# Optimization experiments

Measured on AMD Instinct MI355X. Metric: run time of the kernel, lower is better.

The kernel has to match this reference:

```python
import jax, jax.numpy as jnp
import numpy as np

N_ATOM = 2048
C_ATOM = 128
C_PAIR = 16
N_HEADS = 4
BLOCK = 128
EPS = 1e-5


def _layernorm(x):
    mu = jnp.mean(x, axis=-1, keepdims=True)
    var = jnp.mean(jnp.square(x - mu), axis=-1, keepdims=True)
    return (x - mu) / jnp.sqrt(var + EPS)


def setup_inputs() -> dict:
    key = jax.random.key(0)
    ks = jax.random.split(key, 12)
    s = 0.02
    x = jax.random.normal(ks[0], (N_ATOM, C_ATOM), jnp.float32)
    pair_emb = jax.random.normal(ks[1], (N_ATOM, N_ATOM, C_PAIR), jnp.float32)
    block_index = jax.random.randint(ks[2], (N_ATOM, BLOCK), 0, N_ATOM, jnp.int64)
    Wq = jax.random.normal(ks[3], (C_ATOM, C_ATOM), jnp.float32) * s
    Wk = jax.random.normal(ks[4], (C_ATOM, C_ATOM), jnp.float32) * s
    Wv = jax.random.normal(ks[5], (C_ATOM, C_ATOM), jnp.float32) * s
    Wb = jax.random.normal(ks[6], (N_HEADS, 1), jnp.float32) * s  # nn.Linear(1, num_heads)
    Wout = jax.random.normal(ks[7], (C_ATOM, C_ATOM), jnp.float32) * s
    W1 = jax.random.normal(ks[8], (4 * C_ATOM, C_ATOM), jnp.float32) * s
    b1 = jnp.zeros((4 * C_ATOM,), jnp.float32)
    W2 = jax.random.normal(ks[9], (C_ATOM, 4 * C_ATOM), jnp.float32) * s
    b2 = jnp.zeros((C_ATOM,), jnp.float32)
    return {"x": x, "pair_emb": pair_emb, "block_index": block_index,
            "Wq": Wq, "Wk": Wk, "Wv": Wv, "Wb": Wb, "Wout": Wout,
            "W1": W1, "b1": b1, "W2": W2, "b2": b2}


def reference(x, pair_emb, block_index, Wq, Wk, Wv, Wb, Wout, W1, b1, W2, b2):
    N = x.shape[0]
    d_head = C_ATOM // N_HEADS
    h = _layernorm(x)
    q = (h @ Wq.T).reshape(N, N_HEADS, d_head)
    k = (h @ Wk.T).reshape(N, N_HEADS, d_head)
    v = (h @ Wv.T).reshape(N, N_HEADS, d_head)

    # pair bias per head: mean over c_pair, then Linear(1 -> n_heads)
    pair_mean = jnp.mean(pair_emb, axis=-1)              # [N, N]
    pair_bias = pair_mean[..., None] * Wb[:, 0]          # [N, N, H]

    # local block-sparse attention: each query i attends to keys block_index[i]
    k_g = k[block_index]                                 # [N, B, H, d]
    v_g = v[block_index]                                 # [N, B, H, d]
    rows = jnp.arange(N)[:, None]
    bias = pair_bias[rows, block_index]                  # [N, B, H]

    scale = 1.0 / jnp.sqrt(jnp.asarray(d_head, q.dtype))
    scores = jnp.einsum('nhd,nbhd->nhb', q, k_g) * scale + jnp.transpose(bias, (0, 2, 1))
    attn = jax.nn.softmax(scores, axis=-1)               # [N, H, B]
    attn_out = jnp.einsum('nhb,nbhd->nhd', attn, v_g).reshape(N, C_ATOM)

    x = x + attn_out @ Wout.T
    h2 = _layernorm(x)
    mlp = jax.nn.silu(h2 @ W1.T + b1) @ W2.T + b2
    return x + mlp
```

## Files before the change

### kernel.cpp

```cpp
#include <hip/hip_runtime.h>
#include <hip/hip_bf16.h>

#define N_ATOMS 2048
#define C_DIM   128
#define C_PAIR  16
#define BLK_K   128
#define LN_EPS  1e-5f

typedef float f32x4 __attribute__((ext_vector_type(4)));
typedef short s16x8 __attribute__((ext_vector_type(8)));

__device__ __forceinline__ float bf_lo(unsigned int p) {
    union { unsigned int i; float f; } u; u.i = p << 16; return u.f;
}
__device__ __forceinline__ float bf_hi(unsigned int p) {
    union { unsigned int i; float f; } u; u.i = p & 0xffff0000u; return u.f;
}
__device__ __forceinline__ float bf2f(unsigned short s) {
    union { unsigned int i; float f; } u; u.i = ((unsigned int)s) << 16; return u.f;
}
__device__ __forceinline__ unsigned short f2bf(float f) {
    union { float f; unsigned int i; } u; u.f = f;
    const unsigned int r = u.i + 0x7fffu + ((u.i >> 16) & 1u);
    return (unsigned short)(r >> 16);
}

__device__ __forceinline__ s16x8 lda_frag(const unsigned short* base,
                                          int rowBytes, int kstep, int lane) {
    const int m    = lane & 15;
    const int koff = kstep * 64 + ((lane >> 4) << 4);
    const int addr = m * rowBytes + (koff ^ ((m & 7) << 4));
    return *reinterpret_cast<const s16x8*>(
        reinterpret_cast<const char*>(base) + addr);
}

__device__ void pack_unit(int u, int lane,
                          const float* __restrict__ Wout,
                          const float* __restrict__ W1,
                          const float* __restrict__ W2,
                          unsigned short* __restrict__ WoutP,
                          unsigned short* __restrict__ W1P,
                          unsigned short* __restrict__ W2P)
{
    const float* W; unsigned short* P; int K, local;
    if (u < 32)       { W = Wout; P = WoutP; K = 128; local = u; }
    else if (u < 160) { W = W1;   P = W1P;   K = 128; local = u - 32; }
    else              { W = W2;   P = W2P;   K = 512; local = u - 160; }
    const int ksteps = K >> 5;
    const int ntile  = local / ksteps;
    const int kstep  = local - ntile * ksteps;
    const int n  = ntile * 16 + (lane & 15);
    const int k0 = kstep * 32 + ((lane >> 4) << 3);
    const float4* src = reinterpret_cast<const float4*>(W + (size_t)n * K + k0);
    const float4 a = src[0], b = src[1];
    s16x8 o;
    o[0] = (short)f2bf(a.x); o[1] = (short)f2bf(a.y);
    o[2] = (short)f2bf(a.z); o[3] = (short)f2bf(a.w);
    o[4] = (short)f2bf(b.x); o[5] = (short)f2bf(b.y);
    o[6] = (short)f2bf(b.z); o[7] = (short)f2bf(b.w);
    reinterpret_cast<s16x8*>(P)[local * 64 + lane] = o;
}

__global__ __launch_bounds__(512) void ln_qkv_kernel(
    const float* __restrict__ x,
    const float* __restrict__ Wq, const float* __restrict__ Wk,
    const float* __restrict__ Wv,
    const float* __restrict__ Wout, const float* __restrict__ W1,
    const float* __restrict__ W2,
    float* __restrict__ q,
    unsigned short* __restrict__ kb, unsigned short* __restrict__ vb,
    unsigned short* __restrict__ WoutP, unsigned short* __restrict__ W1P,
    unsigned short* __restrict__ W2P)
{
    __shared__ __align__(16) unsigned short hB[16][128];
    const int t = threadIdx.x;
    const int bid = blockIdx.x;
    const int row0 = bid * 16;

    if (t < 64)       pack_unit(bid * 2,     t,       Wout, W1, W2, WoutP, W1P, W2P);
    else if (t < 128) pack_unit(bid * 2 + 1, t - 64,  Wout, W1, W2, WoutP, W1P, W2P);
    else if (t < 192 && bid < 32)
                      pack_unit(256 + bid,   t - 128, Wout, W1, W2, WoutP, W1P, W2P);

    {
        const int r = t >> 5, l = t & 31;
        const float4 xv = reinterpret_cast<const float4*>(
            x + (size_t)(row0 + r) * C_DIM)[l];
        float s  = xv.x + xv.y + xv.z + xv.w;
        float ss = xv.x*xv.x + xv.y*xv.y + xv.z*xv.z + xv.w*xv.w;
        #pragma unroll
        for (int m = 16; m >= 1; m >>= 1) {
            s  += __shfl_xor(s,  m);
            ss += __shfl_xor(ss, m);
        }
        const float mu  = s * (1.0f / 128.0f);
        const float var = ss * (1.0f / 128.0f) - mu * mu;
        const float inv = rsqrtf(var + LN_EPS);
        union { unsigned long long u64; unsigned short u16[4]; } pk;
        pk.u16[0] = f2bf((xv.x - mu) * inv);
        pk.u16[1] = f2bf((xv.y - mu) * inv);
        pk.u16[2] = f2bf((xv.z - mu) * inv);
        pk.u16[3] = f2bf((xv.w - mu) * inv);
        *reinterpret_cast<unsigned long long*>(
            reinterpret_cast<char*>(&hB[0][0]) +
            r * 256 + ((l * 8) ^ ((r & 7) << 4))) = pk.u64;
    }
    __syncthreads();

    {
        const int wv = t >> 6, lane = t & 63;
        s16x8 afr[4];
        #pragma unroll
        for (int ks = 0; ks < 4; ++ks) afr[ks] = lda_frag(&hB[0][0], 256, ks, lane);

        const int n = wv * 16 + (lane & 15);
        #pragma unroll
        for (int p = 0; p < 3; ++p) {
            const float* W = (p == 0) ? Wq : (p == 1) ? Wk : Wv;
            f32x4 acc = {0.f, 0.f, 0.f, 0.f};
            #pragma unroll
            for (int ks = 0; ks < 4; ++ks) {
                const int k0 = ks * 32 + ((lane >> 4) << 3);
                const float4* src = reinterpret_cast<const float4*>(
                    W + (size_t)n * C_DIM + k0);
                const float4 a = src[0], b = src[1];
                s16x8 bfr;
                bfr[0] = (short)f2bf(a.x); bfr[1] = (short)f2bf(a.y);
                bfr[2] = (short)f2bf(a.z); bfr[3] = (short)f2bf(a.w);
                bfr[4] = (short)f2bf(b.x); bfr[5] = (short)f2bf(b.y);
                bfr[6] = (short)f2bf(b.z); bfr[7] = (short)f2bf(b.w);
                acc = __builtin_amdgcn_mfma_f32_16x16x32_bf16(afr[ks], bfr, acc, 0, 0, 0);
            }
            #pragma unroll
            for (int ii = 0; ii < 4; ++ii) {
                const int m = ((lane >> 4) << 2) + ii;
                const size_t off = (size_t)(row0 + m) * C_DIM + n;
                if (p == 0)      q[off]  = acc[ii];
                else if (p == 1) kb[off] = f2bf(acc[ii]);
                else             vb[off] = f2bf(acc[ii]);
            }
        }
    }
}

__global__ __launch_bounds__(512, 4) void attn_mlp_kernel(
    const float* __restrict__ q, const unsigned short* __restrict__ kb,
    const unsigned short* __restrict__ vb, const float* __restrict__ pair,
    const int*  __restrict__ bidx, const float* __restrict__ Wb,
    const float* __restrict__ x,
    const unsigned short* __restrict__ WoutP,
    const unsigned short* __restrict__ W1P, const float* __restrict__ b1,
    const unsigned short* __restrict__ W2P, const float* __restrict__ b2,
    float* __restrict__ out)
{
    __shared__ __align__(16) float qS[4][128];
    __shared__ __align__(16) int   idxS[4][128];
    __shared__ __align__(16) float S[4][4][128];
    __shared__ __align__(16) float ys[4][128];
    __shared__ __align__(16) unsigned short aoB[16][128];
    __shared__ __align__(16) unsigned short h2B[16][128];
    __shared__ __align__(16) unsigned short gsB[16][512];

    const int t = threadIdx.x;
    const int row0 = blockIdx.x * 4;
    const int r = t >> 7;
    const int u = t & 127;
    const int row = row0 + r;
    const int wv = t >> 6, lane = t & 63;

    const int j = bidx[(size_t)row * BLK_K + u];
    idxS[r][u] = j;
    qS[r][u] = q[(size_t)row * C_DIM + u];
    if (t < 128) {
        const int r2 = t >> 5, l = t & 31;
        const float4 xv = reinterpret_cast<const float4*>(
            x + (size_t)(row0 + r2) * C_DIM)[l];
        *reinterpret_cast<float4*>(&ys[r2][l * 4]) = xv;
    }
    {
        const uint4 z = {0,0,0,0};
        #pragma unroll
        for (int s = t; s < 192; s += 512)
            reinterpret_cast<uint4*>(&aoB[4][0])[s] = z;
        #pragma unroll
        for (int s = t; s < 192; s += 512)
            reinterpret_cast<uint4*>(&h2B[4][0])[s] = z;
        for (int s = t; s < 768; s += 512)
            reinterpret_cast<uint4*>(&gsB[4][0])[s] = z;
    }
    const f32x4* pr = reinterpret_cast<const f32x4*>(
        pair + ((size_t)row * N_ATOMS + (size_t)j) * C_PAIR);
    const f32x4 p0 = __builtin_nontemporal_load(pr + 0);
    const f32x4 p1 = __builtin_nontemporal_load(pr + 1);
    const f32x4 p2 = __builtin_nontemporal_load(pr + 2);
    const f32x4 p3 = __builtin_nontemporal_load(pr + 3);
    __syncthreads();

    {
        const uint4* kr = reinterpret_cast<const uint4*>(kb + (size_t)j * C_DIM);
        const float4* q4 = reinterpret_cast<const float4*>(&qS[r][0]);
        float sc[4];
        #pragma unroll
        for (int h = 0; h < 4; ++h) {
            float a = 0.f;
            #pragma unroll
            for (int d = 0; d < 4; ++d) {
                const uint4  kk = kr[h * 4 + d];
                const float4 qa = q4[h * 8 + d * 2];
                const float4 qc = q4[h * 8 + d * 2 + 1];
                a += bf_lo(kk.x)*qa.x + bf_hi(kk.x)*qa.y
                   + bf_lo(kk.y)*qa.z + bf_hi(kk.y)*qa.w;
                a += bf_lo(kk.z)*qc.x + bf_hi(kk.z)*qc.y
                   + bf_lo(kk.w)*qc.z + bf_hi(kk.w)*qc.w;
            }
            sc[h] = a;
        }
        const float pm = (p0.x+p0.y+p0.z+p0.w + p1.x+p1.y+p1.z+p1.w +
                          p2.x+p2.y+p2.z+p2.w + p3.x+p3.y+p3.z+p3.w) * (1.0f/16.0f);
        const float scale = 0.17677669529663687f;
        #pragma unroll
        for (int h = 0; h < 4; ++h)
            S[r][h][u] = sc[h] * scale + pm * Wb[h];
    }
    __syncthreads();

    {
        const int g = u >> 5, l = u & 31;
        const float v0 = S[r][g][l],      v1 = S[r][g][l + 32],
                    v2 = S[r][g][l + 64], v3 = S[r][g][l + 96];
        float mx = fmaxf(fmaxf(v0, v1), fmaxf(v2, v3));
        #pragma unroll
        for (int m = 16; m >= 1; m >>= 1) mx = fmaxf(mx, __shfl_xor(mx, m));
        const float e0 = __expf(v0 - mx), e1 = __expf(v1 - mx),
                    e2 = __expf(v2 - mx), e3 = __expf(v3 - mx);
        float sm = e0 + e1 + e2 + e3;
        #pragma unroll
        for (int m = 16; m >= 1; m >>= 1) sm += __shfl_xor(sm, m);
        const float rs = 1.0f / sm;
        S[r][g][l]      = e0 * rs;
        S[r][g][l + 32] = e1 * rs;
        S[r][g][l + 64] = e2 * rs;
        S[r][g][l + 96] = e3 * rs;
    }
    __syncthreads();

    {
        const int hh = u >> 5;
        const float4* Sv = reinterpret_cast<const float4*>(&S[r][hh][0]);
        const int4*   iv = reinterpret_cast<const int4*>(&idxS[r][0]);
        float acc = 0.f;
        #pragma unroll 8
        for (int bq = 0; bq < 32; ++bq) {
            const float4 s4 = Sv[bq];
            const int4   j4 = iv[bq];
            acc += s4.x * bf2f(vb[(size_t)j4.x * C_DIM + u]);
            acc += s4.y * bf2f(vb[(size_t)j4.y * C_DIM + u]);
            acc += s4.z * bf2f(vb[(size_t)j4.z * C_DIM + u]);
            acc += s4.w * bf2f(vb[(size_t)j4.w * C_DIM + u]);
        }
        *reinterpret_cast<unsigned short*>(
            reinterpret_cast<char*>(&aoB[0][0]) +
            r * 256 + (((u * 2)) ^ ((r & 7) << 4))) = f2bf(acc);
    }
    __syncthreads();

    {
        f32x4 acc = {0.f, 0.f, 0.f, 0.f};
        const s16x8* Bp = reinterpret_cast<const s16x8*>(WoutP);
        #pragma unroll
        for (int ks = 0; ks < 4; ++ks) {
            const s16x8 a = lda_frag(&aoB[0][0], 256, ks, lane);
            const s16x8 b = Bp[(wv * 4 + ks) * 64 + lane];
            acc = __builtin_amdgcn_mfma_f32_16x16x32_bf16(a, b, acc, 0, 0, 0);
        }
        if (lane < 32) {
            const int c = wv * 16 + (lane & 15);
            #pragma unroll
            for (int i = 0; i < 4; ++i) {
                const int m = ((lane >> 4) << 2) + i;
                if (m < 4) ys[m][c] += acc[i];
            }
        }
    }
    __syncthreads();

    if (t < 128) {
        const int rr = t >> 5, l = t & 31;
        const float4 yv = *reinterpret_cast<const float4*>(&ys[rr][l * 4]);
        float s  = yv.x + yv.y + yv.z + yv.w;
        float ss = yv.x*yv.x + yv.y*yv.y + yv.z*yv.z + yv.w*yv.w;
        #pragma unroll
        for (int m = 16; m >= 1; m >>= 1) {
            s  += __shfl_xor(s,  m);
            ss += __shfl_xor(ss, m);
        }
        const float mu  = s * (1.0f / 128.0f);
        const float var = ss * (1.0f / 128.0f) - mu * mu;
        const float inv = rsqrtf(var + LN_EPS);
        union { unsigned long long u64; unsigned short u16[4]; } pk;
        pk.u16[0] = f2bf((yv.x - mu) * inv);
        pk.u16[1] = f2bf((yv.y - mu) * inv);
        pk.u16[2] = f2bf((yv.z - mu) * inv);
        pk.u16[3] = f2bf((yv.w - mu) * inv);
        *reinterpret_cast<unsigned long long*>(
            reinterpret_cast<char*>(&h2B[0][0]) +
            rr * 256 + ((l * 8) ^ ((rr & 7) << 4))) = pk.u64;
    }
    __syncthreads();

    {
        s16x8 afr[4];
        #pragma unroll
        for (int ks = 0; ks < 4; ++ks) afr[ks] = lda_frag(&h2B[0][0], 256, ks, lane);
        const s16x8* Bp = reinterpret_cast<const s16x8*>(W1P);
        #pragma unroll
        for (int tt = 0; tt < 4; ++tt) {
            const int tile = wv * 4 + tt;
            f32x4 acc = {0.f, 0.f, 0.f, 0.f};
            #pragma unroll
            for (int ks = 0; ks < 4; ++ks) {
                const s16x8 b = Bp[(tile * 4 + ks) * 64 + lane];
                acc = __builtin_amdgcn_mfma_f32_16x16x32_bf16(afr[ks], b, acc, 0, 0, 0);
            }
            if (lane < 32) {
                const int c = tile * 16 + (lane & 15);
                const float bb = b1[c];
                #pragma unroll
                for (int i = 0; i < 4; ++i) {
                    const int m = ((lane >> 4) << 2) + i;
                    if (m < 4) {
                        const float g = acc[i] + bb;
                        const float sv = g / (1.0f + __expf(-g));
                        *reinterpret_cast<unsigned short*>(
                            reinterpret_cast<char*>(&gsB[0][0]) +
                            m * 1024 + ((c * 2) ^ ((m & 7) << 4))) = f2bf(sv);
                    }
                }
            }
        }
    }
    __syncthreads();

    {
        f32x4 acc = {0.f, 0.f, 0.f, 0.f};
        const s16x8* Bp = reinterpret_cast<const s16x8*>(W2P);
        #pragma unroll
        for (int ks = 0; ks < 16; ++ks) {
            const s16x8 a = lda_frag(&gsB[0][0], 1024, ks, lane);
            const s16x8 b = Bp[(wv * 16 + ks) * 64 + lane];
            acc = __builtin_amdgcn_mfma_f32_16x16x32_bf16(a, b, acc, 0, 0, 0);
        }
        if (lane < 32) {
            const int c = wv * 16 + (lane & 15);
            const float bb = b2[c];
            #pragma unroll
            for (int i = 0; i < 4; ++i) {
                const int m = ((lane >> 4) << 2) + i;
                if (m < 4)
                    out[(size_t)(row0 + m) * C_DIM + c] = ys[m][c] + bb + acc[i];
            }
        }
    }
}

extern "C" void kernel_launch(void* const* d_in, const int* in_sizes, int n_in,
                              void* d_out, int out_size, void* d_ws, size_t ws_size,
                              hipStream_t stream)
{
    const float* x    = (const float*)d_in[0];
    const float* pair = (const float*)d_in[1];
    const int*   bidx = (const int*)  d_in[2];
    const float* Wq   = (const float*)d_in[3];
    const float* Wk   = (const float*)d_in[4];
    const float* Wv   = (const float*)d_in[5];
    const float* Wb   = (const float*)d_in[6];
    const float* Wout = (const float*)d_in[7];
    const float* W1   = (const float*)d_in[8];
    const float* b1   = (const float*)d_in[9];
    const float* W2   = (const float*)d_in[10];
    const float* b2   = (const float*)d_in[11];
    float* out = (float*)d_out;

    char* ws = (char*)d_ws;
    float*          q     = (float*)ws;
    unsigned short* kb    = (unsigned short*)(ws + (1 << 20));
    unsigned short* vb    = (unsigned short*)(ws + (1 << 20) + (1 << 19));
    unsigned short* WoutP = (unsigned short*)(ws + (2 << 20));
    unsigned short* W1P   = (unsigned short*)(ws + (2 << 20) + (32 << 10));
    unsigned short* W2P   = (unsigned short*)(ws + (2 << 20) + (160 << 10));

    hipLaunchKernelGGL(ln_qkv_kernel, dim3(N_ATOMS / 16), dim3(512), 0, stream,
                       x, Wq, Wk, Wv, Wout, W1, W2, q, kb, vb, WoutP, W1P, W2P);
    hipLaunchKernelGGL(attn_mlp_kernel, dim3(N_ATOMS / 4), dim3(512), 0, stream,
                       q, kb, vb, pair, bidx, Wb, x, WoutP, W1P, b1, W2P, b2, out);
}
```

Before: 45.59 us.

## Split fused attention+MLP kernel into separate attention and 16-row MLP kernels

The fused attention/MLP kernel is split in two. An attention kernel runs one row per 128-thread block and writes bf16 attention output to workspace. An MLP kernel then processes 16 rows per block, so the 16x16 MFMA tiles are fully used instead of 4 of 16 rows wasting three quarters of the matrix work. This costs an extra launch and a global round trip for the attention output, but removes the wasted MFMA work and the redundant weight reads per 4-row block.

Result: slower. 47.54 us (+4.3%).

```diff
diff --git a/kernel.cpp b/kernel.cpp
--- a/kernel.cpp
+++ b/kernel.cpp
@@ -143,51 +143,23 @@
     }
 }
 
-__global__ __launch_bounds__(512, 4) void attn_mlp_kernel(
+__global__ __launch_bounds__(128) void attn_kernel(
     const float* __restrict__ q, const unsigned short* __restrict__ kb,
     const unsigned short* __restrict__ vb, const float* __restrict__ pair,
     const int*  __restrict__ bidx, const float* __restrict__ Wb,
-    const float* __restrict__ x,
-    const unsigned short* __restrict__ WoutP,
-    const unsigned short* __restrict__ W1P, const float* __restrict__ b1,
-    const unsigned short* __restrict__ W2P, const float* __restrict__ b2,
-    float* __restrict__ out)
-{
-    __shared__ __align__(16) float qS[4][128];
-    __shared__ __align__(16) int   idxS[4][128];
-    __shared__ __align__(16) float S[4][4][128];
-    __shared__ __align__(16) float ys[4][128];
-    __shared__ __align__(16) unsigned short aoB[16][128];
-    __shared__ __align__(16) unsigned short h2B[16][128];
-    __shared__ __align__(16) unsigned short gsB[16][512];
-
-    const int t = threadIdx.x;
-    const int row0 = blockIdx.x * 4;
-    const int r = t >> 7;
-    const int u = t & 127;
-    const int row = row0 + r;
-    const int wv = t >> 6, lane = t & 63;
-
-    const int j = bidx[(size_t)row * BLK_K + u];
-    idxS[r][u] = j;
-    qS[r][u] = q[(size_t)row * C_DIM + u];
-    if (t < 128) {
-        const int r2 = t >> 5, l = t & 31;
-        const float4 xv = reinterpret_cast<const float4*>(
-            x + (size_t)(row0 + r2) * C_DIM)[l];
-        *reinterpret_cast<float4*>(&ys[r2][l * 4]) = xv;
-    }
-    {
-        const uint4 z = {0,0,0,0};
-        #pragma unroll
-        for (int s = t; s < 192; s += 512)
-            reinterpret_cast<uint4*>(&aoB[4][0])[s] = z;
-        #pragma unroll
-        for (int s = t; s < 192; s += 512)
-            reinterpret_cast<uint4*>(&h2B[4][0])[s] = z;
-        for (int s = t; s < 768; s += 512)
-            reinterpret_cast<uint4*>(&gsB[4][0])[s] = z;
-    }
+    unsigned short* __restrict__ ao)
+{
+    __shared__ __align__(16) float qS[128];
+    __shared__ __align__(16) int   idxS[128];
+    __shared__ __align__(16) float S[4][128];
+
+    const int t   = threadIdx.x;
+    const int row = blockIdx.x;
+
+    const int j = bidx[(size_t)row * BLK_K + t];
+    idxS[t] = j;
+    qS[t] = q[(size_t)row * C_DIM + t];
+
     const f32x4* pr = reinterpret_cast<const f32x4*>(
         pair + ((size_t)row * N_ATOMS + (size_t)j) * C_PAIR);
     const f32x4 p0 = __builtin_nontemporal_load(pr + 0);
@@ -198,7 +170,7 @@
 
     {
         const uint4* kr = reinterpret_cast<const uint4*>(kb + (size_t)j * C_DIM);
-        const float4* q4 = reinterpret_cast<const float4*>(&qS[r][0]);
+        const float4* q4 = reinterpret_cast<const float4*>(qS);
         float sc[4];
         #pragma unroll
         for (int h = 0; h < 4; ++h) {
@@ -220,14 +192,14 @@
         const float scale = 0.17677669529663687f;
         #pragma unroll
         for (int h = 0; h < 4; ++h)
-            S[r][h][u] = sc[h] * scale + pm * Wb[h];
-    }
-    __syncthreads();
-
-    {
-        const int g = u >> 5, l = u & 31;
-        const float v0 = S[r][g][l],      v1 = S[r][g][l + 32],
-                    v2 = S[r][g][l + 64], v3 = S[r][g][l + 96];
+            S[h][t] = sc[h] * scale + pm * Wb[h];
+    }
+    __syncthreads();
+
+    {
+        const int g = t >> 5, l = t & 31;
+        const float v0 = S[g][l], v1 = S[g][l + 32],
+                    v2 = S[g][l + 64], v3 = S[g][l + 96];
         float mx = fmaxf(fmaxf(v0, v1), fmaxf(v2, v3));
         #pragma unroll
         for (int m = 16; m >= 1; m >>= 1) mx = fmaxf(mx, __shfl_xor(mx, m));
@@ -237,30 +209,57 @@
         #pragma unroll
         for (int m = 16; m >= 1; m >>= 1) sm += __shfl_xor(sm, m);
         const float rs = 1.0f / sm;
-        S[r][g][l]      = e0 * rs;
-        S[r][g][l + 32] = e1 * rs;
-        S[r][g][l + 64] = e2 * rs;
-        S[r][g][l + 96] = e3 * rs;
-    }
-    __syncthreads();
-
-    {
-        const int hh = u >> 5;
-        const float4* Sv = reinterpret_cast<const float4*>(&S[r][hh][0]);
-        const int4*   iv = reinterpret_cast<const int4*>(&idxS[r][0]);
+        S[g][l]      = e0 * rs;
+        S[g][l + 32] = e1 * rs;
+        S[g][l + 64] = e2 * rs;
+        S[g][l + 96] = e3 * rs;
+    }
+    __syncthreads();
+
+    {
+        const int hh = t >> 5;
+        const float4* Sv = reinterpret_cast<const float4*>(&S[hh][0]);
+        const int4*   iv = reinterpret_cast<const int4*>(idxS);
         float acc = 0.f;
         #pragma unroll 8
         for (int bq = 0; bq < 32; ++bq) {
             const float4 s4 = Sv[bq];
             const int4   j4 = iv[bq];
-            acc += s4.x * bf2f(vb[(size_t)j4.x * C_DIM + u]);
-            acc += s4.y * bf2f(vb[(size_t)j4.y * C_DIM + u]);
-            acc += s4.z * bf2f(vb[(size_t)j4.z * C_DIM + u]);
-            acc += s4.w * bf2f(vb[(size_t)j4.w * C_DIM + u]);
-        }
-        *reinterpret_cast<unsigned short*>(
+            acc += s4.x * bf2f(vb[(size_t)j4.x * C_DIM + t]);
+            acc += s4.y * bf2f(vb[(size_t)j4.y * C_DIM + t]);
+            acc += s4.z * bf2f(vb[(size_t)j4.z * C_DIM + t]);
+            acc += s4.w * bf2f(vb[(size_t)j4.w * C_DIM + t]);
+        }
+        ao[(size_t)row * C_DIM + t] = f2bf(acc);
+    }
+}
+
+__global__ __launch_bounds__(512) void mlp_kernel(
+    const unsigned short* __restrict__ ao, const float* __restrict__ x,
+    const unsigned short* __restrict__ WoutP,
+    const unsigned short* __restrict__ W1P, const float* __restrict__ b1,
+    const unsigned short* __restrict__ W2P, const float* __restrict__ b2,
+    float* __restrict__ out)
+{
+    __shared__ __align__(16) unsigned short aoB[16][128];
+    __shared__ __align__(16) float ys[16][128];
+    __shared__ __align__(16) unsigned short h2B[16][128];
+    __shared__ __align__(16) unsigned short gsB[16][512];
+
+    const int t = threadIdx.x;
+    const int row0 = blockIdx.x * 16;
+    const int wv = t >> 6, lane = t & 63;
+
+    {
+        const int m = t >> 5, g = t & 31;
+        const unsigned long long v = *reinterpret_cast<const unsigned long long*>(
+            ao + (size_t)(row0 + m) * C_DIM + g * 4);
+        *reinterpret_cast<unsigned long long*>(
             reinterpret_cast<char*>(&aoB[0][0]) +
-            r * 256 + (((u * 2)) ^ ((r & 7) << 4))) = f2bf(acc);
+            m * 256 + ((g * 8) ^ ((m & 7) << 4))) = v;
+        const float4 xv = reinterpret_cast<const float4*>(
+            x + (size_t)(row0 + m) * C_DIM)[g];
+        *reinterpret_cast<float4*>(&ys[m][g * 4]) = xv;
     }
     __syncthreads();
 
@@ -273,18 +272,16 @@
             const s16x8 b = Bp[(wv * 4 + ks) * 64 + lane];
             acc = __builtin_amdgcn_mfma_f32_16x16x32_bf16(a, b, acc, 0, 0, 0);
         }
-        if (lane < 32) {
-            const int c = wv * 16 + (lane & 15);
-            #pragma unroll
-            for (int i = 0; i < 4; ++i) {
-                const int m = ((lane >> 4) << 2) + i;
-                if (m < 4) ys[m][c] += acc[i];
-            }
-        }
-    }
-    __syncthreads();
-
-    if (t < 128) {
+        const int c = wv * 16 + (lane & 15);
+        #pragma unroll
+        for (int i = 0; i < 4; ++i) {
+            const int m = ((lane >> 4) << 2) + i;
+            ys[m][c] += acc[i];
+        }
+    }
+    __syncthreads();
+
+    {
         const int rr = t >> 5, l = t & 31;
         const float4 yv = *reinterpret_cast<const float4*>(&ys[rr][l * 4]);
         float s  = yv.x + yv.y + yv.z + yv.w;
@@ -322,20 +319,16 @@
                 const s16x8 b = Bp[(tile * 4 + ks) * 64 + lane];
                 acc = __builtin_amdgcn_mfma_f32_16x16x32_bf16(afr[ks], b, acc, 0, 0, 0);
             }
-            if (lane < 32) {
-                const int c = tile * 16 + (lane & 15);
-                const float bb = b1[c];
-                #pragma unroll
-                for (int i = 0; i < 4; ++i) {
-                    const int m = ((lane >> 4) << 2) + i;
-                    if (m < 4) {
-                        const float g = acc[i] + bb;
-                        const float sv = g / (1.0f + __expf(-g));
-                        *reinterpret_cast<unsigned short*>(
-                            reinterpret_cast<char*>(&gsB[0][0]) +
-                            m * 1024 + ((c * 2) ^ ((m & 7) << 4))) = f2bf(sv);
-                    }
-                }
+            const int c = tile * 16 + (lane & 15);
+            const float bb = b1[c];
+            #pragma unroll
+            for (int i = 0; i < 4; ++i) {
+                const int m = ((lane >> 4) << 2) + i;
+                const float g = acc[i] + bb;
+                const float sv = g / (1.0f + __expf(-g));
+                *reinterpret_cast<unsigned short*>(
+                    reinterpret_cast<char*>(&gsB[0][0]) +
+                    m * 1024 + ((c * 2) ^ ((m & 7) << 4))) = f2bf(sv);
             }
         }
     }
@@ -350,15 +343,12 @@
             const s16x8 b = Bp[(wv * 16 + ks) * 64 + lane];
             acc = __builtin_amdgcn_mfma_f32_16x16x32_bf16(a, b, acc, 0, 0, 0);
         }
-        if (lane < 32) {
-            const int c = wv * 16 + (lane & 15);
-            const float bb = b2[c];
-            #pragma unroll
-            for (int i = 0; i < 4; ++i) {
-                const int m = ((lane >> 4) << 2) + i;
-                if (m < 4)
-                    out[(size_t)(row0 + m) * C_DIM + c] = ys[m][c] + bb + acc[i];
-            }
+        const int c = wv * 16 + (lane & 15);
+        const float bb = b2[c];
+        #pragma unroll
+        for (int i = 0; i < 4; ++i) {
+            const int m = ((lane >> 4) << 2) + i;
+            out[(size_t)(row0 + m) * C_DIM + c] = ys[m][c] + bb + acc[i];
         }
     }
 }
@@ -385,12 +375,15 @@
     float*          q     = (float*)ws;
     unsigned short* kb    = (unsigned short*)(ws + (1 << 20));
     unsigned short* vb    = (unsigned short*)(ws + (1 << 20) + (1 << 19));
-    unsigned short* WoutP = (unsigned short*)(ws + (2 << 20));
-    unsigned short* W1P   = (unsigned short*)(ws + (2 << 20) + (32 << 10));
-    unsigned short* W2P   = (unsigned short*)(ws + (2 << 20) + (160 << 10));
+    unsigned short* ao    = (unsigned short*)(ws + (2 << 20));
+    unsigned short* WoutP = (unsigned short*)(ws + (2 << 20) + (1 << 19));
+    unsigned short* W1P   = (unsigned short*)(ws + (2 << 20) + (1 << 19) + (32 << 10));
+    unsigned short* W2P   = (unsigned short*)(ws + (2 << 20) + (1 << 19) + (160 << 10));
 
     hipLaunchKernelGGL(ln_qkv_kernel, dim3(N_ATOMS / 16), dim3(512), 0, stream,
                        x, Wq, Wk, Wv, Wout, W1, W2, q, kb, vb, WoutP, W1P, W2P);
-    hipLaunchKernelGGL(attn_mlp_kernel, dim3(N_ATOMS / 4), dim3(512), 0, stream,
-                       q, kb, vb, pair, bidx, Wb, x, WoutP, W1P, b1, W2P, b2, out);
-}
+    hipLaunchKernelGGL(attn_kernel, dim3(N_ATOMS), dim3(128), 0, stream,
+                       q, kb, vb, pair, bidx, Wb, ao);
+    hipLaunchKernelGGL(mlp_kernel, dim3(N_ATOMS / 16), dim3(512), 0, stream,
+                       ao, x, WoutP, W1P, b1, W2P, b2, out);
+}
```
